# Kernel tuning notes

Measured on AMD Instinct MI355X. Metric: run time of the kernel, lower is better.

The kernel has to match this reference:

```python
import jax, jax.numpy as jnp
import numpy as np

B, N, F_IN, H, S = 8, 2048, 128, 128, 2
ALPHA = 0.1  # LeakyReLU slope


def setup_inputs() -> dict:
    key = jax.random.key(0)
    ks = jax.random.split(key, 10)
    X_bt = jax.random.normal(ks[0], (B, N, F_IN), dtype=jnp.float32)
    distance_matrix = jax.random.uniform(ks[1], (N, N), dtype=jnp.float32)
    sigmas = jnp.array([0.2, 1.0], dtype=jnp.float32)  # GaussianKernelGenerator scales[:2]
    # Per-scale GeoGATLayer params (stacked on leading scale dim)
    W_w = jax.random.normal(ks[2], (S, H, F_IN), dtype=jnp.float32) * (1.0 / np.sqrt(F_IN))
    W_b = jnp.zeros((S, H), dtype=jnp.float32)
    # attn_fc: Linear(2H, 1) split into the two halves acting on h_i and h_j
    a_i = jax.random.normal(ks[3], (S, H), dtype=jnp.float32) * (1.0 / np.sqrt(2 * H))
    a_j = jax.random.normal(ks[4], (S, H), dtype=jnp.float32) * (1.0 / np.sqrt(2 * H))
    a_b = jnp.zeros((S,), dtype=jnp.float32)
    thr = jnp.full((S,), 0.3, dtype=jnp.float32)
    fus_w = jax.random.normal(ks[5], (H, S * H), dtype=jnp.float32) * (1.0 / np.sqrt(S * H))
    fus_b = jnp.zeros((H,), dtype=jnp.float32)
    return {"X_bt": X_bt, "distance_matrix": distance_matrix, "sigmas": sigmas,
            "W_w": W_w, "W_b": W_b, "a_i": a_i, "a_j": a_j, "a_b": a_b,
            "thr": thr, "fus_w": fus_w, "fus_b": fus_b}


def _leaky_relu(x):
    return jnp.where(x >= 0, x, ALPHA * x)


def reference(X_bt, distance_matrix, sigmas, W_w, W_b, a_i, a_j, a_b, thr, fus_w, fus_b):
    n = distance_matrix.shape[0]
    # layer clones dist and sets diag=1.0 (only for the 1/d additive bias)
    dist_diag1 = distance_matrix.at[jnp.diag_indices(n)].set(1.0)
    inv_d = 1.0 / (dist_diag1 + 1e-5)  # (N,N)
    outs = []
    for s in range(S):
        h = jnp.einsum('bnf,hf->bnh', X_bt, W_w[s]) + W_b[s]  # (B,N,H)
        # attn_fc(cat(h_i,h_j)) == h_i@a_i + h_j@a_j + bias (no concat materialized)
        si = h @ a_i[s]  # (B,N)
        sj = h @ a_j[s]  # (B,N)
        e = _leaky_relu(si[:, :, None] + sj[:, None, :] + a_b[s])  # (B,N,N)
        e = e + inv_d[None]
        A = jnp.exp(-distance_matrix ** 2 / (2.0 * sigmas[s] ** 2))  # Gaussian kernel
        mask = jax.nn.sigmoid(10.0 * (A - thr[s]))
        e = e * mask[None]
        attn = jax.nn.softmax(e, axis=-1)  # dropout is identity in eval
        outs.append(jnp.einsum('bnm,bmh->bnh', attn, h))
    H_cat = jnp.concatenate(outs, axis=-1)  # (B,N,S*H)
    return jnp.einsum('bnk,hk->bnh', H_cat, fus_w) + fus_b
```

## Files before the change

kernel.cpp:

```cpp
#include <hip/hip_runtime.h>
#include <cstdint>
#include <cstddef>

#define BB 8
#define NN 2048
#define FF 128
#define HH 128
#define SS 2

typedef _Float16 f16x8 __attribute__((ext_vector_type(8)));
typedef _Float16 f16x4 __attribute__((ext_vector_type(4)));
typedef float f32x4 __attribute__((ext_vector_type(4)));

__global__ void k0_proj(const float* __restrict__ Ww, const float* __restrict__ Wb,
                        const float* __restrict__ ai, const float* __restrict__ aj,
                        const float* __restrict__ ab,
                        float* __restrict__ w_ai, float* __restrict__ w_aj,
                        float* __restrict__ cst)
{
    const int t = threadIdx.x;
    const int s = t >> 7, f = t & 127;
    const float* wp = Ww + (size_t)s * HH * FF + f;
    const float* aip = ai + s * HH;
    const float* ajp = aj + s * HH;
    float accI = 0.f, accJ = 0.f;
    for (int c = 0; c < HH; ++c) {
        float w = wp[(size_t)c * FF];
        accI = fmaf(w, aip[c], accI);
        accJ = fmaf(w, ajp[c], accJ);
    }
    w_ai[s * FF + f] = accI;
    w_aj[s * FF + f] = accJ;
    if (t < 2 * SS) {
        int ss = t & 1; bool isI = t < 2;
        const float* av = (isI ? ai : aj) + ss * HH;
        const float* wb = Wb + ss * HH;
        float c = 0.f;
        for (int k = 0; k < HH; ++k) c = fmaf(wb[k], av[k], c);
        if (isI) c += ab[ss];
        cst[t] = c;
    }
}

__global__ __launch_bounds__(256) void geo_kernel(
    const float* __restrict__ dist, const float* __restrict__ sigmas,
    const float* __restrict__ thr, _Float16* __restrict__ g1, float* __restrict__ g2)
{
    const size_t idx = ((size_t)blockIdx.x * 256 + threadIdx.x) * 8;
    const int s = (int)(idx >> 22);
    const int i = (int)((idx >> 11) & (NN - 1));
    const int j0 = (int)(idx & (NN - 1));
    const float sg = sigmas[s];
    const float inv2s2 = 1.0f / (2.0f * sg * sg);
    const float th = thr[s];
    const float* dp = dist + (size_t)i * NN + j0;
    float4 d0 = *(const float4*)dp, d1 = *(const float4*)(dp + 4);
    float dv[8] = {d0.x, d0.y, d0.z, d0.w, d1.x, d1.y, d1.z, d1.w};
    f16x8 o1; float og[8];
    #pragma unroll
    for (int k = 0; k < 8; ++k) {
        float d = dv[k];
        float A = __expf(-d * d * inv2s2);
        float msk = 1.0f / (1.0f + __expf(-10.0f * (A - th)));
        float dd = (j0 + k == i) ? 1.0f : d;
        float invd = 1.0f / (dd + 1e-5f);
        o1[k] = (_Float16)msk;
        og[k] = msk * invd;
    }
    *(f16x8*)(g1 + idx) = o1;
    *(float4*)(g2 + idx)     = (float4){og[0], og[1], og[2], og[3]};
    *(float4*)(g2 + idx + 4) = (float4){og[4], og[5], og[6], og[7]};
}

__global__ __launch_bounds__(256, 2) void prep_kernel(
    const float* __restrict__ X, const float* __restrict__ Ww, const float* __restrict__ Wb,
    const float* __restrict__ w_ai, const float* __restrict__ w_aj, const float* __restrict__ cst,
    _Float16* __restrict__ h_t, float* __restrict__ srow, float* __restrict__ scol)
{
    const int s = blockIdx.z, b = blockIdx.y;
    const int n0 = blockIdx.x * 64;
    const int tid = threadIdx.x;
    __shared__ __align__(16) unsigned char smem[49152];

    {
        const int r = tid >> 2, fq = tid & 3;
        const float* src = X + ((size_t)b * NN + n0 + r) * FF + fq * 32;
        unsigned char* dst = smem + r * 256;
        const unsigned rs = r & 15;
        #pragma unroll
        for (int k = 0; k < 4; ++k) {
            float4 v0 = *(const float4*)(src + k * 8);
            float4 v1 = *(const float4*)(src + k * 8 + 4);
            f16x8 h;
            h[0] = (_Float16)v0.x; h[1] = (_Float16)v0.y; h[2] = (_Float16)v0.z; h[3] = (_Float16)v0.w;
            h[4] = (_Float16)v1.x; h[5] = (_Float16)v1.y; h[6] = (_Float16)v1.z; h[7] = (_Float16)v1.w;
            *(f16x8*)(dst + (((fq * 4 + k) ^ rs) << 4)) = h;
        }
    }
    {
        const int ch = tid >> 1, kh8 = (tid & 1) * 8;
        const float* src = Ww + ((size_t)s * HH + ch) * FF + kh8 * 8;
        unsigned char* dst = smem + 16384 + ch * 256;
        const unsigned cs = ch & 15;
        #pragma unroll
        for (int k = 0; k < 8; ++k) {
            float4 v0 = *(const float4*)(src + k * 8);
            float4 v1 = *(const float4*)(src + k * 8 + 4);
            f16x8 h;
            h[0] = (_Float16)v0.x; h[1] = (_Float16)v0.y; h[2] = (_Float16)v0.z; h[3] = (_Float16)v0.w;
            h[4] = (_Float16)v1.x; h[5] = (_Float16)v1.y; h[6] = (_Float16)v1.z; h[7] = (_Float16)v1.w;
            *(f16x8*)(dst + (((kh8 + k) ^ cs) << 4)) = h;
        }
    }
    __syncthreads();

    const int wave = tid >> 6, lane = tid & 63;
    const int lm = lane & 15, lq = lane >> 4, rbase = lq * 4;
    f32x4 acc[4][2];
    #pragma unroll
    for (int m = 0; m < 4; ++m)
        #pragma unroll
        for (int n = 0; n < 2; ++n) acc[m][n] = (f32x4){0.f, 0.f, 0.f, 0.f};

    #pragma unroll
    for (int ks = 0; ks < 4; ++ks) {
        f16x8 af[4], bf[2];
        #pragma unroll
        for (int m = 0; m < 4; ++m) {
            int r = m * 16 + lm;
            af[m] = *(const f16x8*)(smem + r * 256 + ((((ks << 2) | lq) ^ (r & 15)) << 4));
        }
        #pragma unroll
        for (int n = 0; n < 2; ++n) {
            int ch = wave * 32 + n * 16 + lm;
            bf[n] = *(const f16x8*)(smem + 16384 + ch * 256 + ((((ks << 2) | lq) ^ (ch & 15)) << 4));
        }
        #pragma unroll
        for (int m = 0; m < 4; ++m)
            #pragma unroll
            for (int n = 0; n < 2; ++n)
                acc[m][n] = __builtin_amdgcn_mfma_f32_16x16x32_f16(af[m], bf[n], acc[m][n], 0, 0, 0);
    }
    {
        float wb0 = Wb[s * HH + wave * 32 + lm];
        float wb1 = Wb[s * HH + wave * 32 + 16 + lm];
        #pragma unroll
        for (int m = 0; m < 4; ++m)
            #pragma unroll
            for (int n = 0; n < 2; ++n) {
                float wb = n ? wb1 : wb0;
                f16x4 hv;
                #pragma unroll
                for (int r = 0; r < 4; ++r) hv[r] = (_Float16)(acc[m][n][r] + wb);
                int ch = wave * 32 + n * 16 + lm;
                *(f16x4*)(h_t + ((size_t)((s * BB + b) * HH + ch)) * NN + n0 + m * 16 + rbase) = hv;
            }
    }
    {
        const int r = tid >> 2, q = tid & 3;
        const unsigned char* xrow = smem + r * 256;
        const unsigned rs = r & 15;
        const float* wi = w_ai + s * FF + q * 32;
        const float* wj = w_aj + s * FF + q * 32;
        float pi = 0.f, pj = 0.f;
        #pragma unroll
        for (int k = 0; k < 4; ++k) {
            f16x8 xv = *(const f16x8*)(xrow + (((q * 4 + k) ^ rs) << 4));
            float4 wi0 = *(const float4*)(wi + k * 8), wi1 = *(const float4*)(wi + k * 8 + 4);
            float4 wj0 = *(const float4*)(wj + k * 8), wj1 = *(const float4*)(wj + k * 8 + 4);
            pi += (float)xv[0]*wi0.x + (float)xv[1]*wi0.y + (float)xv[2]*wi0.z + (float)xv[3]*wi0.w
                + (float)xv[4]*wi1.x + (float)xv[5]*wi1.y + (float)xv[6]*wi1.z + (float)xv[7]*wi1.w;
            pj += (float)xv[0]*wj0.x + (float)xv[1]*wj0.y + (float)xv[2]*wj0.z + (float)xv[3]*wj0.w
                + (float)xv[4]*wj1.x + (float)xv[5]*wj1.y + (float)xv[6]*wj1.z + (float)xv[7]*wj1.w;
        }
        pi += __shfl_xor(pi, 1); pi += __shfl_xor(pi, 2);
        pj += __shfl_xor(pj, 1); pj += __shfl_xor(pj, 2);
        if (q == 0) {
            size_t idx = (size_t)(s * BB + b) * NN + n0 + r;
            srow[idx] = pi + cst[s];
            scol[idx] = pj + cst[2 + s];
        }
    }
}

template<bool GEO>
__global__ __launch_bounds__(256, 4) void attn_kernel(
    const float* __restrict__ dist, const float* __restrict__ sigmas,
    const float* __restrict__ thr, const _Float16* __restrict__ h_t,
    const float* __restrict__ srow, const float* __restrict__ scol,
    const _Float16* __restrict__ g1, const float* __restrict__ g2,
    _Float16* __restrict__ Hcat)
{
    const int s = blockIdx.z, b = blockIdx.y;
    const int i0 = blockIdx.x * 32;
    const int tid = threadIdx.x;

    __shared__ __align__(16) unsigned char smem[37248];
    float* m_row  = (float*)(smem + 36864);
    float* l_row  = (float*)(smem + 36864 + 128);
    float* sc_row = (float*)(smem + 36864 + 256);

    const size_t sb = (size_t)(s * BB + b) * NN;
    const _Float16* hbase = h_t + (size_t)(s * BB + b) * HH * NN;

    float inv2s2 = 0.f, th = 0.f;
    if (!GEO) {
        float sg = sigmas[s];
        inv2s2 = 1.0f / (2.0f * sg * sg);
        th = thr[s];
    }

    if (tid < 32) { m_row[tid] = -INFINITY; l_row[tid] = 0.f; }

    f32x4 acc[2][2];
    #pragma unroll
    for (int m = 0; m < 2; ++m)
        #pragma unroll
        for (int n = 0; n < 2; ++n) acc[m][n] = (f32x4){0.f, 0.f, 0.f, 0.f};

    const int wave = tid >> 6, lane = tid & 63;
    const int lm = lane & 15, lq = lane >> 4, rbase = lq * 4;
    const int chq = wave;

    const int row = tid >> 3, jg = tid & 7;
    const int gi = i0 + row;
    const float si = srow[sb + gi];
    const size_t girow = GEO ? ((size_t)s * NN + gi) * NN : (size_t)gi * NN;

    __syncthreads();

    for (int jt = 0; jt < NN / 64; ++jt) {
        const int j0 = jt * 64;
        const int jb = j0 + jg * 8;
        float e[8];
        {
            float4 c0 = *(const float4*)(scol + sb + jb);
            float4 c1 = *(const float4*)(scol + sb + jb + 4);
            float cv[8] = {c0.x, c0.y, c0.z, c0.w, c1.x, c1.y, c1.z, c1.w};
            if (GEO) {
                f16x8 gv = *(const f16x8*)(g1 + girow + jb);
                float4 q0 = *(const float4*)(g2 + girow + jb);
                float4 q1 = *(const float4*)(g2 + girow + jb + 4);
                float gg[8] = {q0.x, q0.y, q0.z, q0.w, q1.x, q1.y, q1.z, q1.w};
                #pragma unroll
                for (int k = 0; k < 8; ++k) {
                    float t = si + cv[k];
                    float lr = fmaxf(t, 0.1f * t);
                    e[k] = fmaf(lr, (float)gv[k], gg[k]);
                }
            } else {
                float4 d0 = *(const float4*)(dist + girow + jb);
                float4 d1 = *(const float4*)(dist + girow + jb + 4);
                float dv[8] = {d0.x, d0.y, d0.z, d0.w, d1.x, d1.y, d1.z, d1.w};
                #pragma unroll
                for (int k = 0; k < 8; ++k) {
                    float d = dv[k];
                    float A = __expf(-d * d * inv2s2);
                    float den = 1.0f + __expf(-10.0f * (A - th));
                    float r1 = __builtin_amdgcn_rcpf(den); r1 = r1 * (2.0f - den * r1);
                    float dd = (jb + k == gi) ? 1.0f : d;
                    float x2 = dd + 1e-5f;
                    float ri = __builtin_amdgcn_rcpf(x2); ri = ri * (2.0f - x2 * ri);
                    float t = si + cv[k];
                    float lr = fmaxf(t, 0.1f * t);
                    e[k] = (lr + ri) * r1;
                }
            }
        }
        float mt = fmaxf(fmaxf(fmaxf(e[0], e[1]), fmaxf(e[2], e[3])),
                         fmaxf(fmaxf(e[4], e[5]), fmaxf(e[6], e[7])));
        mt = fmaxf(mt, __shfl_xor(mt, 1));
        mt = fmaxf(mt, __shfl_xor(mt, 2));
        mt = fmaxf(mt, __shfl_xor(mt, 4));
        const float m_old = m_row[row];
        const float m_new = fmaxf(m_old, mt);
        float psum = 0.f;
        f16x8 pv;
        #pragma unroll
        for (int k = 0; k < 8; ++k) {
            float p = __expf(e[k] - m_new);
            psum += p;
            pv[k] = (_Float16)p;
        }
        psum += __shfl_xor(psum, 1);
        psum += __shfl_xor(psum, 2);
        psum += __shfl_xor(psum, 4);
        *(f16x8*)(smem + row * 128 + ((jg * 16) ^ ((row & 7) << 4))) = pv;
        if (jg == 0) {
            float scl = __expf(m_old - m_new);
            m_row[row] = m_new;
            sc_row[row] = scl;
            l_row[row] = l_row[row] * scl + psum;
        }
        {
            const int ch = tid >> 1, hf = tid & 1;
            const _Float16* hsrc = hbase + (size_t)ch * NN + j0 + hf * 32;
            unsigned char* hdst = smem + 4096 + ch * 256;
            const unsigned cs = ch & 15;
            #pragma unroll
            for (int q = 0; q < 4; ++q) {
                f16x8 v = *(const f16x8*)(hsrc + q * 8);
                *(f16x8*)(hdst + (((hf * 4 + q) ^ cs) << 4)) = v;
            }
        }
        __syncthreads();
        {
            f16x8 af[2][2], bf[2][2];
            #pragma unroll
            for (int m = 0; m < 2; ++m) {
                int r = m * 16 + lm;
                unsigned sw = (r & 7) << 4;
                af[m][0] = *(const f16x8*)(smem + r * 128 + ((lq * 16) ^ sw));
                af[m][1] = *(const f16x8*)(smem + r * 128 + ((64 + lq * 16) ^ sw));
            }
            #pragma unroll
            for (int n = 0; n < 2; ++n) {
                int ch = chq * 32 + n * 16 + lm;
                const unsigned cs = ch & 15;
                bf[n][0] = *(const f16x8*)(smem + 4096 + ch * 256 + ((lq ^ cs) << 4));
                bf[n][1] = *(const f16x8*)(smem + 4096 + ch * 256 + (((4 | lq) ^ cs) << 4));
            }
            #pragma unroll
            for (int m = 0; m < 2; ++m) {
                f32x4 scv = *(const f32x4*)&sc_row[m * 16 + rbase];
                #pragma unroll
                for (int n = 0; n < 2; ++n) {
                    acc[m][n] *= scv;
                    acc[m][n] = __builtin_amdgcn_mfma_f32_16x16x32_f16(af[m][0], bf[n][0], acc[m][n], 0, 0, 0);
                    acc[m][n] = __builtin_amdgcn_mfma_f32_16x16x32_f16(af[m][1], bf[n][1], acc[m][n], 0, 0, 0);
                }
            }
        }
        __syncthreads();
    }

    _Float16* ebuf = (_Float16*)smem;
    #pragma unroll
    for (int m = 0; m < 2; ++m) {
        f32x4 lv = *(const f32x4*)&l_row[m * 16 + rbase];
        f32x4 inv;
        #pragma unroll
        for (int r = 0; r < 4; ++r) inv[r] = __builtin_amdgcn_rcpf(lv[r]);
        #pragma unroll
        for (int n = 0; n < 2; ++n)
            #pragma unroll
            for (int r = 0; r < 4; ++r)
                ebuf[(m * 16 + rbase + r) * 128 + chq * 32 + n * 16 + lm] =
                    (_Float16)(acc[m][n][r] * inv[r]);
    }
    __syncthreads();
    {
        const int r = tid >> 3, c0 = (tid & 7) * 16;
        f16x8 v0 = *(const f16x8*)(ebuf + r * 128 + c0);
        f16x8 v1 = *(const f16x8*)(ebuf + r * 128 + c0 + 8);
        _Float16* dst = Hcat + ((size_t)(b * NN + i0 + r)) * (SS * HH) + s * HH + c0;
        *(f16x8*)dst = v0;
        *(f16x8*)(dst + 8) = v1;
    }
}

__global__ __launch_bounds__(256, 2) void fuse_kernel(
    const _Float16* __restrict__ Hcat, const float* __restrict__ fw,
    const float* __restrict__ fb, float* __restrict__ out)
{
    const int r0 = blockIdx.x * 64;
    const int tid = threadIdx.x;
    __shared__ __align__(16) unsigned char smem[65536];

    {
        const int r = tid >> 2, q = tid & 3;
        const _Float16* src = Hcat + (size_t)(r0 + r) * 256 + q * 64;
        unsigned char* dst = smem + r * 512;
        const unsigned rs = r & 7;
        #pragma unroll
        for (int k = 0; k < 8; ++k) {
            f16x8 v = *(const f16x8*)(src + k * 8);
            *(f16x8*)(dst + (((q * 8 + k) ^ rs) << 4)) = v;
        }
    }

    const int wave = tid >> 6, lane = tid & 63;
    const int lm = lane & 15, lq = lane >> 4, rbase = lq * 4;
    f32x4 acc[4][2];
    #pragma unroll
    for (int m = 0; m < 4; ++m)
        #pragma unroll
        for (int n = 0; n < 2; ++n) acc[m][n] = (f32x4){0.f, 0.f, 0.f, 0.f};

    for (int c = 0; c < 2; ++c) {
        __syncthreads();
        {
            const int ch = tid >> 1, kh8 = (tid & 1) * 8;
            const float* src = fw + (size_t)ch * 256 + c * 128 + kh8 * 8;
            unsigned char* dst = smem + 32768 + ch * 256;
            const unsigned cs = ch & 15;
            #pragma unroll
            for (int k = 0; k < 8; ++k) {
                float4 v0 = *(const float4*)(src + k * 8);
                float4 v1 = *(const float4*)(src + k * 8 + 4);
                f16x8 h;
                h[0] = (_Float16)v0.x; h[1] = (_Float16)v0.y; h[2] = (_Float16)v0.z; h[3] = (_Float16)v0.w;
                h[4] = (_Float16)v1.x; h[5] = (_Float16)v1.y; h[6] = (_Float16)v1.z; h[7] = (_Float16)v1.w;
                *(f16x8*)(dst + (((kh8 + k) ^ cs) << 4)) = h;
            }
        }
        __syncthreads();
        #pragma unroll
        for (int ks = 0; ks < 4; ++ks) {
            const int gks = c * 4 + ks;
            f16x8 af[4], bf[2];
            #pragma unroll
            for (int m = 0; m < 4; ++m) {
                int r = m * 16 + lm;
                af[m] = *(const f16x8*)(smem + r * 512 + ((((gks << 2) | lq) ^ (r & 7)) << 4));
            }
            #pragma unroll
            for (int n = 0; n < 2; ++n) {
                int ch = wave * 32 + n * 16 + lm;
                bf[n] = *(const f16x8*)(smem + 32768 + ch * 256 + ((((ks << 2) | lq) ^ (ch & 15)) << 4));
            }
            #pragma unroll
            for (int m = 0; m < 4; ++m)
                #pragma unroll
                for (int n = 0; n < 2; ++n)
                    acc[m][n] = __builtin_amdgcn_mfma_f32_16x16x32_f16(af[m], bf[n], acc[m][n], 0, 0, 0);
        }
    }
    {
        float fb0 = fb[wave * 32 + lm];
        float fb1 = fb[wave * 32 + 16 + lm];
        #pragma unroll
        for (int m = 0; m < 4; ++m)
            #pragma unroll
            for (int n = 0; n < 2; ++n) {
                float fbv = n ? fb1 : fb0;
                int ch = wave * 32 + n * 16 + lm;
                #pragma unroll
                for (int r = 0; r < 4; ++r)
                    out[(size_t)(r0 + m * 16 + rbase + r) * HH + ch] = acc[m][n][r] + fbv;
            }
    }
}

extern "C" void kernel_launch(void* const* d_in, const int* in_sizes, int n_in,
                              void* d_out, int out_size, void* d_ws, size_t ws_size,
                              hipStream_t stream)
{
    const float* X      = (const float*)d_in[0];
    const float* dist   = (const float*)d_in[1];
    const float* sigmas = (const float*)d_in[2];
    const float* Ww     = (const float*)d_in[3];
    const float* Wb     = (const float*)d_in[4];
    const float* ai     = (const float*)d_in[5];
    const float* aj     = (const float*)d_in[6];
    const float* ab     = (const float*)d_in[7];
    const float* thr    = (const float*)d_in[8];
    const float* fw     = (const float*)d_in[9];
    const float* fb     = (const float*)d_in[10];
    float* out = (float*)d_out;

    char* ws = (char*)d_ws;
    float*     w_ai = (float*)(ws);
    float*     w_aj = (float*)(ws + 1024);
    float*     cst  = (float*)(ws + 2048);
    float*     srow = (float*)(ws + 4096);
    float*     scol = (float*)(ws + 135168);
    _Float16*  h_t  = (_Float16*)(ws + 266240);
    _Float16*  Hcat = (_Float16*)(ws + 8654848);
    _Float16*  g1   = (_Float16*)(ws + 17043456);
    float*     g2   = (float*)(ws + 33820672);
    const bool geo = ws_size >= (size_t)67375104;

    k0_proj<<<1, 256, 0, stream>>>(Ww, Wb, ai, aj, ab, w_ai, w_aj, cst);
    prep_kernel<<<dim3(NN / 64, BB, SS), 256, 0, stream>>>(X, Ww, Wb, w_ai, w_aj, cst, h_t, srow, scol);
    if (geo) {
        geo_kernel<<<(SS * NN * NN / 8) / 256, 256, 0, stream>>>(dist, sigmas, thr, g1, g2);
        attn_kernel<true><<<dim3(NN / 32, BB, SS), 256, 0, stream>>>(
            dist, sigmas, thr, h_t, srow, scol, g1, g2, Hcat);
    } else {
        attn_kernel<false><<<dim3(NN / 32, BB, SS), 256, 0, stream>>>(
            dist, sigmas, thr, h_t, srow, scol, (const _Float16*)nullptr, (const float*)nullptr, Hcat);
    }
    fuse_kernel<<<BB * NN / 64, 256, 0, stream>>>(Hcat, fw, fb, out);
}
```

Before: 192.6 us.

## Pipeline attention loop with register prefetch, fold score projection into prep, retile fuse

The attention kernel is restructured around register-prefetched tiles (LOADT) and double-buffered shared memory, with an online-softmax max/sum kept in registers, so global loads overlap the MFMA work. Its occupancy hint drops from 4 to 3 blocks. The separate k0_proj launch is removed: srow and scol are now computed from the MFMA accumulators in prep_kernel using a shuffle and shared-memory reduction. fuse_kernel is retiled to 32 rows per block, giving more blocks with less shared memory each. The risks are higher register pressure in the attention loop and slightly different rounding for srow and scol, since they are now taken from the fp32 accumulators.

```diff
diff --git a/kernel.cpp b/kernel.cpp
--- a/kernel.cpp
+++ b/kernel.cpp
@@ -7,40 +7,11 @@
 #define FF 128
 #define HH 128
 #define SS 2
+#define NT (NN / 64)
 
 typedef _Float16 f16x8 __attribute__((ext_vector_type(8)));
 typedef _Float16 f16x4 __attribute__((ext_vector_type(4)));
 typedef float f32x4 __attribute__((ext_vector_type(4)));
-
-__global__ void k0_proj(const float* __restrict__ Ww, const float* __restrict__ Wb,
-                        const float* __restrict__ ai, const float* __restrict__ aj,
-                        const float* __restrict__ ab,
-                        float* __restrict__ w_ai, float* __restrict__ w_aj,
-                        float* __restrict__ cst)
-{
-    const int t = threadIdx.x;
-    const int s = t >> 7, f = t & 127;
-    const float* wp = Ww + (size_t)s * HH * FF + f;
-    const float* aip = ai + s * HH;
-    const float* ajp = aj + s * HH;
-    float accI = 0.f, accJ = 0.f;
-    for (int c = 0; c < HH; ++c) {
-        float w = wp[(size_t)c * FF];
-        accI = fmaf(w, aip[c], accI);
-        accJ = fmaf(w, ajp[c], accJ);
-    }
-    w_ai[s * FF + f] = accI;
-    w_aj[s * FF + f] = accJ;
-    if (t < 2 * SS) {
-        int ss = t & 1; bool isI = t < 2;
-        const float* av = (isI ? ai : aj) + ss * HH;
-        const float* wb = Wb + ss * HH;
-        float c = 0.f;
-        for (int k = 0; k < HH; ++k) c = fmaf(wb[k], av[k], c);
-        if (isI) c += ab[ss];
-        cst[t] = c;
-    }
-}
 
 __global__ __launch_bounds__(256) void geo_kernel(
     const float* __restrict__ dist, const float* __restrict__ sigmas,
@@ -74,13 +45,15 @@
 
 __global__ __launch_bounds__(256, 2) void prep_kernel(
     const float* __restrict__ X, const float* __restrict__ Ww, const float* __restrict__ Wb,
-    const float* __restrict__ w_ai, const float* __restrict__ w_aj, const float* __restrict__ cst,
+    const float* __restrict__ ai, const float* __restrict__ aj, const float* __restrict__ ab,
     _Float16* __restrict__ h_t, float* __restrict__ srow, float* __restrict__ scol)
 {
     const int s = blockIdx.z, b = blockIdx.y;
     const int n0 = blockIdx.x * 64;
     const int tid = threadIdx.x;
-    __shared__ __align__(16) unsigned char smem[49152];
+    __shared__ __align__(16) unsigned char smem[51200];
+    float* sredI = (float*)(smem + 49152);
+    float* sredJ = (float*)(smem + 49152 + 1024);
 
     {
         const int r = tid >> 2, fq = tid & 3;
@@ -92,8 +65,8 @@
             float4 v0 = *(const float4*)(src + k * 8);
             float4 v1 = *(const float4*)(src + k * 8 + 4);
             f16x8 h;
-            h[0] = (_Float16)v0.x; h[1] = (_Float16)v0.y; h[2] = (_Float16)v0.z; h[3] = (_Float16)v0.w;
-            h[4] = (_Float16)v1.x; h[5] = (_Float16)v1.y; h[6] = (_Float16)v1.z; h[7] = (_Float16)v1.w;
+            h[0]=(_Float16)v0.x; h[1]=(_Float16)v0.y; h[2]=(_Float16)v0.z; h[3]=(_Float16)v0.w;
+            h[4]=(_Float16)v1.x; h[5]=(_Float16)v1.y; h[6]=(_Float16)v1.z; h[7]=(_Float16)v1.w;
             *(f16x8*)(dst + (((fq * 4 + k) ^ rs) << 4)) = h;
         }
     }
@@ -107,15 +80,15 @@
             float4 v0 = *(const float4*)(src + k * 8);
             float4 v1 = *(const float4*)(src + k * 8 + 4);
             f16x8 h;
-            h[0] = (_Float16)v0.x; h[1] = (_Float16)v0.y; h[2] = (_Float16)v0.z; h[3] = (_Float16)v0.w;
-            h[4] = (_Float16)v1.x; h[5] = (_Float16)v1.y; h[6] = (_Float16)v1.z; h[7] = (_Float16)v1.w;
+            h[0]=(_Float16)v0.x; h[1]=(_Float16)v0.y; h[2]=(_Float16)v0.z; h[3]=(_Float16)v0.w;
+            h[4]=(_Float16)v1.x; h[5]=(_Float16)v1.y; h[6]=(_Float16)v1.z; h[7]=(_Float16)v1.w;
             *(f16x8*)(dst + (((kh8 + k) ^ cs) << 4)) = h;
         }
     }
     __syncthreads();
 
     const int wave = tid >> 6, lane = tid & 63;
-    const int lm = lane & 15, lq = lane >> 4, rbase = lq * 4;
+    const int lm = lane & 15, lq = lane >> 4;
     f32x4 acc[4][2];
     #pragma unroll
     for (int m = 0; m < 4; ++m)
@@ -141,50 +114,64 @@
             for (int n = 0; n < 2; ++n)
                 acc[m][n] = __builtin_amdgcn_mfma_f32_16x16x32_f16(af[m], bf[n], acc[m][n], 0, 0, 0);
     }
-    {
-        float wb0 = Wb[s * HH + wave * 32 + lm];
-        float wb1 = Wb[s * HH + wave * 32 + 16 + lm];
+
+    const float wb0 = Wb[s * HH + wave * 32 + lm];
+    const float wb1 = Wb[s * HH + wave * 32 + 16 + lm];
+    const float ai0 = ai[s * HH + wave * 32 + lm];
+    const float ai1 = ai[s * HH + wave * 32 + 16 + lm];
+    const float aj0 = aj[s * HH + wave * 32 + lm];
+    const float aj1 = aj[s * HH + wave * 32 + 16 + lm];
+    float pI[4][4], pJ[4][4];
+    #pragma unroll
+    for (int m = 0; m < 4; ++m) {
+        #pragma unroll
+        for (int r = 0; r < 4; ++r) {
+            float h0 = acc[m][0][r] + wb0;
+            float h1 = acc[m][1][r] + wb1;
+            pI[m][r] = h0 * ai0 + h1 * ai1;
+            pJ[m][r] = h0 * aj0 + h1 * aj1;
+        }
+        #pragma unroll
+        for (int n = 0; n < 2; ++n) {
+            float wb = n ? wb1 : wb0;
+            f16x4 hv;
+            #pragma unroll
+            for (int r = 0; r < 4; ++r) hv[r] = (_Float16)(acc[m][n][r] + wb);
+            int ch = wave * 32 + n * 16 + lm;
+            *(f16x4*)(h_t + ((size_t)((s * BB + b) * HH + ch)) * NN + n0 + m * 16 + lq * 4) = hv;
+        }
+    }
+    #pragma unroll
+    for (int st = 1; st < 16; st <<= 1) {
         #pragma unroll
         for (int m = 0; m < 4; ++m)
             #pragma unroll
-            for (int n = 0; n < 2; ++n) {
-                float wb = n ? wb1 : wb0;
-                f16x4 hv;
-                #pragma unroll
-                for (int r = 0; r < 4; ++r) hv[r] = (_Float16)(acc[m][n][r] + wb);
-                int ch = wave * 32 + n * 16 + lm;
-                *(f16x4*)(h_t + ((size_t)((s * BB + b) * HH + ch)) * NN + n0 + m * 16 + rbase) = hv;
-            }
-    }
-    {
-        const int r = tid >> 2, q = tid & 3;
-        const unsigned char* xrow = smem + r * 256;
-        const unsigned rs = r & 15;
-        const float* wi = w_ai + s * FF + q * 32;
-        const float* wj = w_aj + s * FF + q * 32;
-        float pi = 0.f, pj = 0.f;
-        #pragma unroll
-        for (int k = 0; k < 4; ++k) {
-            f16x8 xv = *(const f16x8*)(xrow + (((q * 4 + k) ^ rs) << 4));
-            float4 wi0 = *(const float4*)(wi + k * 8), wi1 = *(const float4*)(wi + k * 8 + 4);
-            float4 wj0 = *(const float4*)(wj + k * 8), wj1 = *(const float4*)(wj + k * 8 + 4);
-            pi += (float)xv[0]*wi0.x + (float)xv[1]*wi0.y + (float)xv[2]*wi0.z + (float)xv[3]*wi0.w
-                + (float)xv[4]*wi1.x + (float)xv[5]*wi1.y + (float)xv[6]*wi1.z + (float)xv[7]*wi1.w;
-            pj += (float)xv[0]*wj0.x + (float)xv[1]*wj0.y + (float)xv[2]*wj0.z + (float)xv[3]*wj0.w
-                + (float)xv[4]*wj1.x + (float)xv[5]*wj1.y + (float)xv[6]*wj1.z + (float)xv[7]*wj1.w;
-        }
-        pi += __shfl_xor(pi, 1); pi += __shfl_xor(pi, 2);
-        pj += __shfl_xor(pj, 1); pj += __shfl_xor(pj, 2);
-        if (q == 0) {
-            size_t idx = (size_t)(s * BB + b) * NN + n0 + r;
-            srow[idx] = pi + cst[s];
-            scol[idx] = pj + cst[2 + s];
-        }
+            for (int r = 0; r < 4; ++r) {
+                pI[m][r] += __shfl_xor(pI[m][r], st);
+                pJ[m][r] += __shfl_xor(pJ[m][r], st);
+            }
+    }
+    if (lm == 0) {
+        #pragma unroll
+        for (int m = 0; m < 4; ++m)
+            #pragma unroll
+            for (int r = 0; r < 4; ++r) {
+                sredI[wave * 64 + m * 16 + lq * 4 + r] = pI[m][r];
+                sredJ[wave * 64 + m * 16 + lq * 4 + r] = pJ[m][r];
+            }
+    }
+    __syncthreads();
+    if (tid < 64) {
+        float sI = sredI[tid] + sredI[64 + tid] + sredI[128 + tid] + sredI[192 + tid] + ab[s];
+        float sJ = sredJ[tid] + sredJ[64 + tid] + sredJ[128 + tid] + sredJ[192 + tid];
+        size_t idx = (size_t)(s * BB + b) * NN + n0 + tid;
+        srow[idx] = sI;
+        scol[idx] = sJ;
     }
 }
 
 template<bool GEO>
-__global__ __launch_bounds__(256, 4) void attn_kernel(
+__global__ __launch_bounds__(256, 3) void attn_kernel(
     const float* __restrict__ dist, const float* __restrict__ sigmas,
     const float* __restrict__ thr, const _Float16* __restrict__ h_t,
     const float* __restrict__ srow, const float* __restrict__ scol,
@@ -195,157 +182,176 @@
     const int i0 = blockIdx.x * 32;
     const int tid = threadIdx.x;
 
-    __shared__ __align__(16) unsigned char smem[37248];
-    float* m_row  = (float*)(smem + 36864);
-    float* l_row  = (float*)(smem + 36864 + 128);
-    float* sc_row = (float*)(smem + 36864 + 256);
+    __shared__ __align__(16) unsigned char smem[41344];
+    float* scb    = (float*)(smem + 40960);
+    float* lrow_s = (float*)(smem + 41216);
 
     const size_t sb = (size_t)(s * BB + b) * NN;
     const _Float16* hbase = h_t + (size_t)(s * BB + b) * HH * NN;
 
+    const int wave = tid >> 6, lane = tid & 63;
+    const int lm = lane & 15, lq = lane >> 4;
+    const int chq = wave;
+
+    const int row = tid >> 3, jg = tid & 7, jg8 = jg * 8;
+    const int gi = i0 + row;
+    const unsigned rsw = row & 7;
+    const float si = srow[sb + gi];
+    const size_t girow = ((size_t)s * NN + gi) * NN;
+    const size_t drow = (size_t)gi * NN;
+
+    const int sch = tid >> 1, shf4 = (tid & 1) * 4;
+    const _Float16* hrow = hbase + (size_t)sch * NN + (shf4 >> 2) * 32;
+    const unsigned hsw = sch & 7;
+
     float inv2s2 = 0.f, th = 0.f;
-    if (!GEO) {
-        float sg = sigmas[s];
-        inv2s2 = 1.0f / (2.0f * sg * sg);
-        th = thr[s];
-    }
-
-    if (tid < 32) { m_row[tid] = -INFINITY; l_row[tid] = 0.f; }
+    if (!GEO) { float sg = sigmas[s]; inv2s2 = 1.0f / (2.0f * sg * sg); th = thr[s]; }
 
     f32x4 acc[2][2];
     #pragma unroll
     for (int m = 0; m < 2; ++m)
         #pragma unroll
         for (int n = 0; n < 2; ++n) acc[m][n] = (f32x4){0.f, 0.f, 0.f, 0.f};
-
-    const int wave = tid >> 6, lane = tid & 63;
-    const int lm = lane & 15, lq = lane >> 4, rbase = lq * 4;
-    const int chq = wave;
-
-    const int row = tid >> 3, jg = tid & 7;
-    const int gi = i0 + row;
-    const float si = srow[sb + gi];
-    const size_t girow = GEO ? ((size_t)s * NN + gi) * NN : (size_t)gi * NN;
-
+    float m_r = -3.0e38f, l_r = 0.f;
+
+    f16x8 hA[4], hB[4], gA, gB;
+    f32x4 qA[2], qB[2];
+
+#define LOADT(HT, GT, QT, J0V) {                                              \
+    const _Float16* hp_ = hrow + (J0V);                                       \
+    HT[0] = *(const f16x8*)(hp_);                                             \
+    HT[1] = *(const f16x8*)(hp_ + 8);                                         \
+    HT[2] = *(const f16x8*)(hp_ + 16);                                        \
+    HT[3] = *(const f16x8*)(hp_ + 24);                                        \
+    const int jb_ = (J0V) + jg8;                                              \
+    if (GEO) {                                                                \
+        GT = *(const f16x8*)(g1 + girow + jb_);                               \
+        QT[0] = *(const f32x4*)(g2 + girow + jb_);                            \
+        QT[1] = *(const f32x4*)(g2 + girow + jb_ + 4);                        \
+    } else {                                                                  \
+        (void)GT;                                                             \
+        QT[0] = *(const f32x4*)(dist + drow + jb_);                           \
+        QT[1] = *(const f32x4*)(dist + drow + jb_ + 4);                       \
+    }                                                                         \
+}
+
+#define MFMA_STEP(MB) {                                                       \
+    f16x8 af00, af01, af10, af11, bf00, bf01, bf10, bf11;                     \
+    { const unsigned char* pb_ = smem + (MB) * 4096;                          \
+      int r_ = lm; unsigned sw_ = r_ & 7;                                     \
+      af00 = *(const f16x8*)(pb_ + r_ * 128 + ((lq ^ sw_) << 4));             \
+      af01 = *(const f16x8*)(pb_ + r_ * 128 + (((4 | lq) ^ sw_) << 4));       \
+      r_ = 16 + lm; sw_ = r_ & 7;                                             \
+      af10 = *(const f16x8*)(pb_ + r_ * 128 + ((lq ^ sw_) << 4));             \
+      af11 = *(const f16x8*)(pb_ + r_ * 128 + (((4 | lq) ^ sw_) << 4)); }     \
+    { const unsigned char* hb_ = smem + 8192 + (MB) * 16384;                  \
+      int c_ = chq * 32 + lm; unsigned sw_ = c_ & 7;                          \
+      bf00 = *(const f16x8*)(hb_ + c_ * 128 + ((lq ^ sw_) << 4));             \
+      bf01 = *(const f16x8*)(hb_ + c_ * 128 + (((4 | lq) ^ sw_) << 4));       \
+      c_ = chq * 32 + 16 + lm; sw_ = c_ & 7;                                  \
+      bf10 = *(const f16x8*)(hb_ + c_ * 128 + ((lq ^ sw_) << 4));             \
+      bf11 = *(const f16x8*)(hb_ + c_ * 128 + (((4 | lq) ^ sw_) << 4)); }     \
+    f32x4 sc0 = *(const f32x4*)(scb + (MB) * 32 + lq * 4);                    \
+    f32x4 sc1 = *(const f32x4*)(scb + (MB) * 32 + 16 + lq * 4);               \
+    acc[0][0] *= sc0; acc[0][1] *= sc0;                                       \
+    acc[1][0] *= sc1; acc[1][1] *= sc1;                                       \
+    acc[0][0] = __builtin_amdgcn_mfma_f32_16x16x32_f16(af00, bf00, acc[0][0], 0, 0, 0); \
+    acc[0][0] = __builtin_amdgcn_mfma_f32_16x16x32_f16(af01, bf01, acc[0][0], 0, 0, 0); \
+    acc[0][1] = __builtin_amdgcn_mfma_f32_16x16x32_f16(af00, bf10, acc[0][1], 0, 0, 0); \
+    acc[0][1] = __builtin_amdgcn_mfma_f32_16x16x32_f16(af01, bf11, acc[0][1], 0, 0, 0); \
+    acc[1][0] = __builtin_amdgcn_mfma_f32_16x16x32_f16(af10, bf00, acc[1][0], 0, 0, 0); \
+    acc[1][0] = __builtin_amdgcn_mfma_f32_16x16x32_f16(af11, bf01, acc[1][0], 0, 0, 0); \
+    acc[1][1] = __builtin_amdgcn_mfma_f32_16x16x32_f16(af10, bf10, acc[1][1], 0, 0, 0); \
+    acc[1][1] = __builtin_amdgcn_mfma_f32_16x16x32_f16(af11, bf11, acc[1][1], 0, 0, 0); \
+}
+
+#define PHASE1(HC, GC, QC, J0, PB) {                                          \
+    unsigned char* hd_ = smem + 8192 + (PB) * 16384 + sch * 128;              \
+    *(f16x8*)(hd_ + (((shf4 + 0) ^ hsw) << 4)) = HC[0];                       \
+    *(f16x8*)(hd_ + (((shf4 + 1) ^ hsw) << 4)) = HC[1];                       \
+    *(f16x8*)(hd_ + (((shf4 + 2) ^ hsw) << 4)) = HC[2];                       \
+    *(f16x8*)(hd_ + (((shf4 + 3) ^ hsw) << 4)) = HC[3];                       \
+    const int jb_ = (J0) + jg8;                                               \
+    f32x4 c0_ = *(const f32x4*)(scol + sb + jb_);                             \
+    f32x4 c1_ = *(const f32x4*)(scol + sb + jb_ + 4);                         \
+    float ev[8];                                                              \
+    if (GEO) {                                                                \
+        _Pragma("unroll")                                                     \
+        for (int k = 0; k < 8; ++k) {                                         \
+            float t_ = si + (k < 4 ? c0_[k & 3] : c1_[k & 3]);                \
+            float lr_ = fmaxf(t_, 0.1f * t_);                                 \
+            ev[k] = fmaf(lr_, (float)GC[k], QC[k >> 2][k & 3]);               \
+        }                                                                     \
+    } else {                                                                  \
+        _Pragma("unroll")                                                     \
+        for (int k = 0; k < 8; ++k) {                                         \
+            float d_ = QC[k >> 2][k & 3];                                     \
+            float A_ = __expf(-d_ * d_ * inv2s2);                             \
+            float den_ = 1.0f + __expf(-10.0f * (A_ - th));                   \
+            float r1_ = __builtin_amdgcn_rcpf(den_); r1_ = r1_ * (2.0f - den_ * r1_); \
+            float dd_ = (jb_ + k == gi) ? 1.0f : d_;                          \
+            float x2_ = dd_ + 1e-5f;                                          \
+            float ri_ = __builtin_amdgcn_rcpf(x2_); ri_ = ri_ * (2.0f - x2_ * ri_);   \
+            float t_ = si + (k < 4 ? c0_[k & 3] : c1_[k & 3]);                \
+            float lr_ = fmaxf(t_, 0.1f * t_);                                 \
+            ev[k] = (lr_ + ri_) * r1_;                                        \
+        }                                                                     \
+    }                                                                         \
+    float mt_ = fmaxf(fmaxf(fmaxf(ev[0], ev[1]), fmaxf(ev[2], ev[3])),        \
+                      fmaxf(fmaxf(ev[4], ev[5]), fmaxf(ev[6], ev[7])));       \
+    mt_ = fmaxf(mt_, __shfl_xor(mt_, 1));                                     \
+    mt_ = fmaxf(mt_, __shfl_xor(mt_, 2));                                     \
+    mt_ = fmaxf(mt_, __shfl_xor(mt_, 4));                                     \
+    const float mnew_ = fmaxf(m_r, mt_);                                      \
+    float ps_ = 0.f; f16x8 pv_;                                               \
+    _Pragma("unroll")                                                         \
+    for (int k = 0; k < 8; ++k) {                                             \
+        float p_ = __expf(ev[k] - mnew_);                                     \
+        ps_ += p_; pv_[k] = (_Float16)p_;                                     \
+    }                                                                         \
+    ps_ += __shfl_xor(ps_, 1);                                                \
+    ps_ += __shfl_xor(ps_, 2);                                                \
+    ps_ += __shfl_xor(ps_, 4);                                                \
+    *(f16x8*)(smem + (PB) * 4096 + row * 128 + ((jg ^ rsw) << 4)) = pv_;      \
+    float scl_ = __expf(m_r - mnew_);                                         \
+    if (jg == 0) scb[(PB) * 32 + row] = scl_;                                 \
+    l_r = l_r * scl_ + ps_;                                                   \
+    m_r = mnew_;                                                              \
+}
+
+#define WINDOW(HC, GC, QC, HN, GN, QN, JT, PB, MB) {                          \
+    int jn_ = (JT) + 1; if (jn_ >= NT) jn_ = 0;                               \
+    LOADT(HN, GN, QN, jn_ * 64);                                              \
+    if ((JT) > 0) MFMA_STEP(MB);                                              \
+    PHASE1(HC, GC, QC, (JT) * 64, PB);                                        \
+    __syncthreads();                                                          \
+}
+
+    LOADT(hA, gA, qA, 0);
+    for (int jt = 0; jt < NT; jt += 2) {
+        WINDOW(hA, gA, qA, hB, gB, qB, jt,     0, 1);
+        WINDOW(hB, gB, qB, hA, gA, qA, jt + 1, 1, 0);
+    }
+    if (jg == 0) lrow_s[row] = l_r;
+    MFMA_STEP(1);
     __syncthreads();
 
-    for (int jt = 0; jt < NN / 64; ++jt) {
-        const int j0 = jt * 64;
-        const int jb = j0 + jg * 8;
-        float e[8];
-        {
-            float4 c0 = *(const float4*)(scol + sb + jb);
-            float4 c1 = *(const float4*)(scol + sb + jb + 4);
-            float cv[8] = {c0.x, c0.y, c0.z, c0.w, c1.x, c1.y, c1.z, c1.w};
-            if (GEO) {
-                f16x8 gv = *(const f16x8*)(g1 + girow + jb);
-                float4 q0 = *(const float4*)(g2 + girow + jb);
-                float4 q1 = *(const float4*)(g2 + girow + jb + 4);
-                float gg[8] = {q0.x, q0.y, q0.z, q0.w, q1.x, q1.y, q1.z, q1.w};
-                #pragma unroll
-                for (int k = 0; k < 8; ++k) {
-                    float t = si + cv[k];
-                    float lr = fmaxf(t, 0.1f * t);
-                    e[k] = fmaf(lr, (float)gv[k], gg[k]);
-                }
-            } else {
-                float4 d0 = *(const float4*)(dist + girow + jb);
-                float4 d1 = *(const float4*)(dist + girow + jb + 4);
-                float dv[8] = {d0.x, d0.y, d0.z, d0.w, d1.x, d1.y, d1.z, d1.w};
-                #pragma unroll
-                for (int k = 0; k < 8; ++k) {
-                    float d = dv[k];
-                    float A = __expf(-d * d * inv2s2);
-                    float den = 1.0f + __expf(-10.0f * (A - th));
-                    float r1 = __builtin_amdgcn_rcpf(den); r1 = r1 * (2.0f - den * r1);
-                    float dd = (jb + k == gi) ? 1.0f : d;
-                    float x2 = dd + 1e-5f;
-                    float ri = __builtin_amdgcn_rcpf(x2); ri = ri * (2.0f - x2 * ri);
-                    float t = si + cv[k];
-                    float lr = fmaxf(t, 0.1f * t);
-                    e[k] = (lr + ri) * r1;
-                }
-            }
-        }
-        float mt = fmaxf(fmaxf(fmaxf(e[0], e[1]), fmaxf(e[2], e[3])),
-                         fmaxf(fmaxf(e[4], e[5]), fmaxf(e[6], e[7])));
-        mt = fmaxf(mt, __shfl_xor(mt, 1));
-        mt = fmaxf(mt, __shfl_xor(mt, 2));
-        mt = fmaxf(mt, __shfl_xor(mt, 4));
-        const float m_old = m_row[row];
-        const float m_new = fmaxf(m_old, mt);
-        float psum = 0.f;
-        f16x8 pv;
-        #pragma unroll
-        for (int k = 0; k < 8; ++k) {
-            float p = __expf(e[k] - m_new);
-            psum += p;
-            pv[k] = (_Float16)p;
-        }
-        psum += __shfl_xor(psum, 1);
-        psum += __shfl_xor(psum, 2);
-        psum += __shfl_xor(psum, 4);
-        *(f16x8*)(smem + row * 128 + ((jg * 16) ^ ((row & 7) << 4))) = pv;
-        if (jg == 0) {
-            float scl = __expf(m_old - m_new);
-            m_row[row] = m_new;
-            sc_row[row] = scl;
-            l_row[row] = l_row[row] * scl + psum;
-        }
-        {
-            const int ch = tid >> 1, hf = tid & 1;
-            const _Float16* hsrc = hbase + (size_t)ch * NN + j0 + hf * 32;
-            unsigned char* hdst = smem + 4096 + ch * 256;
-            const unsigned cs = ch & 15;
-            #pragma unroll
-            for (int q = 0; q < 4; ++q) {
-                f16x8 v = *(const f16x8*)(hsrc + q * 8);
-                *(f16x8*)(hdst + (((hf * 4 + q) ^ cs) << 4)) = v;
-            }
-        }
-        __syncthreads();
-        {
-            f16x8 af[2][2], bf[2][2];
-            #pragma unroll
-            for (int m = 0; m < 2; ++m) {
-                int r = m * 16 + lm;
-                unsigned sw = (r & 7) << 4;
-                af[m][0] = *(const f16x8*)(smem + r * 128 + ((lq * 16) ^ sw));
-                af[m][1] = *(const f16x8*)(smem + r * 128 + ((64 + lq * 16) ^ sw));
-            }
-            #pragma unroll
-            for (int n = 0; n < 2; ++n) {
-                int ch = chq * 32 + n * 16 + lm;
-                const unsigned cs = ch & 15;
-                bf[n][0] = *(const f16x8*)(smem + 4096 + ch * 256 + ((lq ^ cs) << 4));
-                bf[n][1] = *(const f16x8*)(smem + 4096 + ch * 256 + (((4 | lq) ^ cs) << 4));
-            }
-            #pragma unroll
-            for (int m = 0; m < 2; ++m) {
-                f32x4 scv = *(const f32x4*)&sc_row[m * 16 + rbase];
-                #pragma unroll
-                for (int n = 0; n < 2; ++n) {
-                    acc[m][n] *= scv;
-                    acc[m][n] = __builtin_amdgcn_mfma_f32_16x16x32_f16(af[m][0], bf[n][0], acc[m][n], 0, 0, 0);
-                    acc[m][n] = __builtin_amdgcn_mfma_f32_16x16x32_f16(af[m][1], bf[n][1], acc[m][n], 0, 0, 0);
-                }
-            }
-        }
-        __syncthreads();
-    }
-
     _Float16* ebuf = (_Float16*)smem;
     #pragma unroll
     for (int m = 0; m < 2; ++m) {
-        f32x4 lv = *(const f32x4*)&l_row[m * 16 + rbase];
+        f32x4 lv = *(const f32x4*)&lrow_s[m * 16 + lq * 4];
         f32x4 inv;
         #pragma unroll
-        for (int r = 0; r < 4; ++r) inv[r] = __builtin_amdgcn_rcpf(lv[r]);
+        for (int r = 0; r < 4; ++r) {
+            float x = lv[r];
+            float iv = __builtin_amdgcn_rcpf(x);
+            inv[r] = iv * (2.0f - x * iv);
+        }
         #pragma unroll
         for (int n = 0; n < 2; ++n)
             #pragma unroll
             for (int r = 0; r < 4; ++r)
-                ebuf[(m * 16 + rbase + r) * 128 + chq * 32 + n * 16 + lm] =
+                ebuf[(m * 16 + lq * 4 + r) * 128 + chq * 32 + n * 16 + lm] =
                     (_Float16)(acc[m][n][r] * inv[r]);
     }
     __syncthreads();
@@ -357,33 +363,37 @@
         *(f16x8*)dst = v0;
         *(f16x8*)(dst + 8) = v1;
     }
+#undef LOADT
+#undef MFMA_STEP
+#undef PHASE1
+#undef WINDOW
 }
 
 __global__ __launch_bounds__(256, 2) void fuse_kernel(
     const _Float16* __restrict__ Hcat, const float* __restrict__ fw,
     const float* __restrict__ fb, float* __restrict__ out)
 {
-    const int r0 = blockIdx.x * 64;
+    const int r0 = blockIdx.x * 32;
     const int tid = threadIdx.x;
-    __shared__ __align__(16) unsigned char smem[65536];
+    __shared__ __align__(16) unsigned char smem[49152];
 
     {
-        const int r = tid >> 2, q = tid & 3;
-        const _Float16* src = Hcat + (size_t)(r0 + r) * 256 + q * 64;
+        const int r = tid >> 3, q = tid & 7;
+        const _Float16* src = Hcat + (size_t)(r0 + r) * 256 + q * 32;
         unsigned char* dst = smem + r * 512;
         const unsigned rs = r & 7;
         #pragma unroll
-        for (int k = 0; k < 8; ++k) {
+        for (int k = 0; k < 4; ++k) {
             f16x8 v = *(const f16x8*)(src + k * 8);
-            *(f16x8*)(dst + (((q * 8 + k) ^ rs) << 4)) = v;
+            *(f16x8*)(dst + (((q * 4 + k) ^ rs) << 4)) = v;
         }
     }
 
     const int wave = tid >> 6, lane = tid & 63;
-    const int lm = lane & 15, lq = lane >> 4, rbase = lq * 4;
-    f32x4 acc[4][2];
-    #pragma unroll
-    for (int m = 0; m < 4; ++m)
+    const int lm = lane & 15, lq = lane >> 4;
+    f32x4 acc[2][2];
+    #pragma unroll
+    for (int m = 0; m < 2; ++m)
         #pragma unroll
         for (int n = 0; n < 2; ++n) acc[m][n] = (f32x4){0.f, 0.f, 0.f, 0.f};
 
@@ -392,15 +402,15 @@
         {
             const int ch = tid >> 1, kh8 = (tid & 1) * 8;
             const float* src = fw + (size_t)ch * 256 + c * 128 + kh8 * 8;
-            unsigned char* dst = smem + 32768 + ch * 256;
+            unsigned char* dst = smem + 16384 + ch * 256;
             const unsigned cs = ch & 15;
             #pragma unroll
             for (int k = 0; k < 8; ++k) {
                 float4 v0 = *(const float4*)(src + k * 8);
                 float4 v1 = *(const float4*)(src + k * 8 + 4);
                 f16x8 h;
-                h[0] = (_Float16)v0.x; h[1] = (_Float16)v0.y; h[2] = (_Float16)v0.z; h[3] = (_Float16)v0.w;
-                h[4] = (_Float16)v1.x; h[5] = (_Float16)v1.y; h[6] = (_Float16)v1.z; h[7] = (_Float16)v1.w;
+                h[0]=(_Float16)v0.x; h[1]=(_Float16)v0.y; h[2]=(_Float16)v0.z; h[3]=(_Float16)v0.w;
+                h[4]=(_Float16)v1.x; h[5]=(_Float16)v1.y; h[6]=(_Float16)v1.z; h[7]=(_Float16)v1.w;
                 *(f16x8*)(dst + (((kh8 + k) ^ cs) << 4)) = h;
             }
         }
@@ -408,19 +418,19 @@
         #pragma unroll
         for (int ks = 0; ks < 4; ++ks) {
             const int gks = c * 4 + ks;
-            f16x8 af[4], bf[2];
-            #pragma unroll
-            for (int m = 0; m < 4; ++m) {
+            f16x8 af[2], bf[2];
+            #pragma unroll
+            for (int m = 0; m < 2; ++m) {
                 int r = m * 16 + lm;
                 af[m] = *(const f16x8*)(smem + r * 512 + ((((gks << 2) | lq) ^ (r & 7)) << 4));
             }
             #pragma unroll
             for (int n = 0; n < 2; ++n) {
                 int ch = wave * 32 + n * 16 + lm;
-                bf[n] = *(const f16x8*)(smem + 32768 + ch * 256 + ((((ks << 2) | lq) ^ (ch & 15)) << 4));
-            }
-            #pragma unroll
-            for (int m = 0; m < 4; ++m)
+                bf[n] = *(const f16x8*)(smem + 16384 + ch * 256 + ((((ks << 2) | lq) ^ (ch & 15)) << 4));
+            }
+            #pragma unroll
+            for (int m = 0; m < 2; ++m)
                 #pragma unroll
                 for (int n = 0; n < 2; ++n)
                     acc[m][n] = __builtin_amdgcn_mfma_f32_16x16x32_f16(af[m], bf[n], acc[m][n], 0, 0, 0);
@@ -430,14 +440,14 @@
         float fb0 = fb[wave * 32 + lm];
         float fb1 = fb[wave * 32 + 16 + lm];
         #pragma unroll
-        for (int m = 0; m < 4; ++m)
+        for (int m = 0; m < 2; ++m)
             #pragma unroll
             for (int n = 0; n < 2; ++n) {
                 float fbv = n ? fb1 : fb0;
                 int ch = wave * 32 + n * 16 + lm;
                 #pragma unroll
                 for (int r = 0; r < 4; ++r)
-                    out[(size_t)(r0 + m * 16 + rbase + r) * HH + ch] = acc[m][n][r] + fbv;
+                    out[(size_t)(r0 + m * 16 + lq * 4 + r) * HH + ch] = acc[m][n][r] + fbv;
             }
     }
 }
@@ -460,19 +470,15 @@
     float* out = (float*)d_out;
 
     char* ws = (char*)d_ws;
-    float*     w_ai = (float*)(ws);
-    float*     w_aj = (float*)(ws + 1024);
-    float*     cst  = (float*)(ws + 2048);
-    float*     srow = (float*)(ws + 4096);
-    float*     scol = (float*)(ws + 135168);
-    _Float16*  h_t  = (_Float16*)(ws + 266240);
-    _Float16*  Hcat = (_Float16*)(ws + 8654848);
-    _Float16*  g1   = (_Float16*)(ws + 17043456);
-    float*     g2   = (float*)(ws + 33820672);
-    const bool geo = ws_size >= (size_t)67375104;
-
-    k0_proj<<<1, 256, 0, stream>>>(Ww, Wb, ai, aj, ab, w_ai, w_aj, cst);
-    prep_kernel<<<dim3(NN / 64, BB, SS), 256, 0, stream>>>(X, Ww, Wb, w_ai, w_aj, cst, h_t, srow, scol);
+    float*     srow = (float*)(ws);
+    float*     scol = (float*)(ws + 131072);
+    _Float16*  h_t  = (_Float16*)(ws + 262144);
+    _Float16*  Hcat = (_Float16*)(ws + 8650752);
+    _Float16*  g1   = (_Float16*)(ws + 17039360);
+    float*     g2   = (float*)(ws + 33816576);
+    const bool geo = ws_size >= (size_t)67371008;
+
+    prep_kernel<<<dim3(NN / 64, BB, SS), 256, 0, stream>>>(X, Ww, Wb, ai, aj, ab, h_t, srow, scol);
     if (geo) {
         geo_kernel<<<(SS * NN * NN / 8) / 256, 256, 0, stream>>>(dist, sigmas, thr, g1, g2);
         attn_kernel<true><<<dim3(NN / 32, BB, SS), 256, 0, stream>>>(
@@ -481,5 +487,5 @@
         attn_kernel<false><<<dim3(NN / 32, BB, SS), 256, 0, stream>>>(
             dist, sigmas, thr, h_t, srow, scol, (const _Float16*)nullptr, (const float*)nullptr, Hcat);
     }
-    fuse_kernel<<<BB * NN / 64, 256, 0, stream>>>(Hcat, fw, fb, out);
-}
+    fuse_kernel<<<BB * NN / 32, 256, 0, stream>>>(Hcat, fw, fb, out);
+}
```

After: 193.9 us. About the same (+0.7%).
